# Kernel optimization log

Measured on AMD Instinct MI355X. Metric: run time of the kernel, lower is better.

Reference implementation:

```python
import jax, jax.numpy as jnp
import numpy as np

B, C, F, NH, DK, DV = 16, 256, 32, 8, 32, 64
S = F * F
EPS = 1e-5
SCALE = DK ** -0.5


def _bn(t, g, b, m, v):
    # t: [B, Ch, H, W]; eval-mode batchnorm with running stats
    inv = g / jnp.sqrt(v + EPS)
    return t * inv[None, :, None, None] + (b - m * inv)[None, :, None, None]


def setup_inputs() -> dict:
    key = jax.random.key(0)
    ks = jax.random.split(key, 24)
    n = lambda i, shape, s=0.05: jax.random.normal(ks[i], shape, jnp.float32) * s
    u = lambda i, shape: jax.random.uniform(ks[i], shape, jnp.float32, 0.5, 1.5)
    # relative-position index table (buffer)
    r = np.arange(F)
    pos = np.stack(np.meshgrid(r, r, indexing='ij'), axis=-1).reshape(-1, 2)
    rel = np.abs(pos[:, None, :] - pos[None, :, :])
    pos_indices = jnp.asarray(rel[..., 0] * F + rel[..., 1], jnp.int32)  # [S, S]
    return {
        'x': jax.random.normal(ks[0], (B, C, F, F), jnp.float32),
        'Wq': n(1, (NH * DK, C)), 'q_g': u(2, (NH * DK,)), 'q_b': n(3, (NH * DK,)), 'q_m': n(4, (NH * DK,)), 'q_v': u(5, (NH * DK,)),
        'Wk': n(6, (NH * DK, C)), 'k_g': u(7, (NH * DK,)), 'k_b': n(8, (NH * DK,)), 'k_m': n(9, (NH * DK,)), 'k_v': u(10, (NH * DK,)),
        'Wv': n(11, (NH * DV, C)), 'v_g': u(12, (NH * DV,)), 'v_b': n(13, (NH * DV,)), 'v_m': n(14, (NH * DV,)), 'v_v': u(15, (NH * DV,)),
        'pos_emb': n(16, (F * F, NH)),
        'Wo': n(17, (C, NH * DV)), 'bo': n(18, (C,)),
        'o_g': u(19, (C,)), 'o_b': n(20, (C,)), 'o_m': n(21, (C,)), 'o_v': u(22, (C,)),
        'pos_indices': pos_indices,
    }


def reference(x, Wq, q_g, q_b, q_m, q_v, Wk, k_g, k_b, k_m, k_v, Wv, v_g, v_b, v_m, v_v,
              pos_emb, Wo, bo, o_g, o_b, o_m, o_v, pos_indices):
    # 1x1 conv == channel GEMM
    q = _bn(jnp.einsum('bchw,oc->bohw', x, Wq), q_g, q_b, q_m, q_v)
    k = _bn(jnp.einsum('bchw,oc->bohw', x, Wk), k_g, k_b, k_m, k_v)
    v = _bn(jnp.einsum('bchw,oc->bohw', x, Wv), v_g, v_b, v_m, v_v)
    # b (n d) h w -> b n s d
    qh = q.reshape(B, NH, DK, S).transpose(0, 1, 3, 2)
    kh = k.reshape(B, NH, DK, S).transpose(0, 1, 3, 2)
    vh = v.reshape(B, NH, DV, S).transpose(0, 1, 3, 2)
    attn = jnp.einsum('bnqd,bnkd->bnqk', qh, kh) * SCALE  # [B, NH, S, S]
    bias = pos_emb[pos_indices]                            # [S, S, NH] gather
    attn = attn + jnp.transpose(bias, (2, 0, 1))[None] / SCALE
    attn = jax.nn.softmax(attn, axis=-1)
    o = jnp.einsum('bnqk,bnkd->bnqd', attn, vh)            # [B, NH, S, DV]
    o = o.transpose(0, 1, 3, 2).reshape(B, NH * DV, F, F)  # b (n d) h w
    o = jax.nn.gelu(o, approximate=False)                  # torch default GELU (erf)
    o = jnp.einsum('bchw,oc->bohw', o, Wo) + bo[None, :, None, None]
    return _bn(o, o_g, o_b, o_m, o_v)
```

## Files before the change

kernel.cpp:

```cpp
#include <hip/hip_runtime.h>

#define B_ 16
#define C_ 256
#define NH_ 8
#define DK_ 32
#define DV_ 64
#define S_ 1024
#define CV_ 512

typedef __bf16 bf16;
typedef bf16 bf16x4 __attribute__((ext_vector_type(4)));
typedef bf16 bf16x8 __attribute__((ext_vector_type(8)));
typedef float f32x4 __attribute__((ext_vector_type(4)));

constexpr float EPSV = 1e-5f;
constexpr float SCALE_ = 0.17677669529663687f;
constexpr float LOG2E_ = 1.4426950408889634f;
constexpr float QSCALE_ = SCALE_ * LOG2E_;
constexpr float BSCALE_ = (1.0f / SCALE_) * LOG2E_;

__global__ void prep_kernel(const float* __restrict__ Wq, const float* __restrict__ qg, const float* __restrict__ qb, const float* __restrict__ qm, const float* __restrict__ qv,
                            const float* __restrict__ Wk, const float* __restrict__ kg, const float* __restrict__ kb, const float* __restrict__ km, const float* __restrict__ kv,
                            const float* __restrict__ Wv, const float* __restrict__ vg, const float* __restrict__ vb, const float* __restrict__ vm, const float* __restrict__ vv,
                            const float* __restrict__ Wo, const float* __restrict__ bo, const float* __restrict__ og_, const float* __restrict__ ob_, const float* __restrict__ om_, const float* __restrict__ ov_,
                            bf16* __restrict__ wqkv, float* __restrict__ bqkv, bf16* __restrict__ wo2, float* __restrict__ bo2) {
  int idx = blockIdx.x * 256 + threadIdx.x;
  if (idx < 1024 * 256) {
    int o = idx >> 8, c = idx & 255;
    float w, g, v;
    if (o < 256)      { w = Wq[o * 256 + c];        g = qg[o];       v = qv[o]; }
    else if (o < 512) { w = Wk[(o - 256) * 256 + c]; g = kg[o - 256]; v = kv[o - 256]; }
    else              { w = Wv[(o - 512) * 256 + c]; g = vg[o - 512]; v = vv[o - 512]; }
    float inv = g * rsqrtf(v + EPSV);
    wqkv[idx] = (bf16)(w * inv);
    if (c == 0) {
      float bb, m;
      if (o < 256)      { bb = qb[o];       m = qm[o]; }
      else if (o < 512) { bb = kb[o - 256]; m = km[o - 256]; }
      else              { bb = vb[o - 512]; m = vm[o - 512]; }
      bqkv[o] = bb - m * inv;
    }
  } else {
    int j = idx - 1024 * 256;
    if (j < 256 * 512) {
      int co = j >> 9, cv = j & 511;
      float inv = og_[co] * rsqrtf(ov_[co] + EPSV);
      wo2[j] = (bf16)(Wo[j] * inv);
      if (cv == 0) bo2[co] = bo[co] * inv + ob_[co] - om_[co] * inv;
    }
  }
}

__global__ __launch_bounds__(256) void xpose_kernel(const float* __restrict__ x, bf16* __restrict__ xT) {
  __shared__ bf16 t[64][66];
  int b = blockIdx.z, c0 = blockIdx.y * 64, s0 = blockIdx.x * 64;
  const float* xp = x + ((size_t)b * C_ + c0) * S_ + s0;
#pragma unroll
  for (int p = 0; p < 4; ++p) {
    int q = p * 256 + threadIdx.x;
    int ci = q >> 4, si4 = (q & 15) * 4;
    float4 v = *(const float4*)(xp + (size_t)ci * S_ + si4);
    t[si4 + 0][ci] = (bf16)v.x;
    t[si4 + 1][ci] = (bf16)v.y;
    t[si4 + 2][ci] = (bf16)v.z;
    t[si4 + 3][ci] = (bf16)v.w;
  }
  __syncthreads();
  bf16* op = xT + ((size_t)b * S_ + s0) * C_ + c0;
#pragma unroll
  for (int p = 0; p < 4; ++p) {
    int q = p * 256 + threadIdx.x;
    int si = q >> 4, ci4 = (q & 15) * 4;
    bf16x4 pk;
#pragma unroll
    for (int e = 0; e < 4; ++e) pk[e] = t[si][ci4 + e];
    *(bf16x4*)(op + (size_t)si * C_ + ci4) = pk;
  }
}

__device__ __forceinline__ void gload16(const void* g, void* l) {
  __builtin_amdgcn_global_load_lds((const __attribute__((address_space(1))) void*)g,
                                   (__attribute__((address_space(3))) void*)l, 16, 0, 0);
}

__global__ __launch_bounds__(256) void qkv_gemm_kernel(const bf16* __restrict__ wqkv, const float* __restrict__ bqkv,
                                                       const bf16* __restrict__ xT, bf16* __restrict__ qh,
                                                       bf16* __restrict__ kh, bf16* __restrict__ vT) {
  __shared__ bf16 alds[2][128 * 32];
  __shared__ bf16 blds[2][128 * 32];
  const int b = blockIdx.z;
  const int ob = blockIdx.y * 128, sb = blockIdx.x * 128;
  const int w = threadIdx.x >> 6, lane = threadIdx.x & 63;
  const int g = lane >> 4, lo = lane & 15;
  const int ow = (w >> 1) * 64, sw = (w & 1) * 64;

  const int r0 = threadIdx.x >> 2, c4 = threadIdx.x & 3;
  const int swz = (c4 ^ ((r0 >> 1) & 3)) * 8;
  const bf16* aS = wqkv + (size_t)(ob + r0) * C_ + swz;
  const bf16* bS = xT + ((size_t)b * S_ + sb + r0) * C_ + swz;
  const int ldst = threadIdx.x * 8;
  auto stage = [&](int buf, int kc) {
    gload16(aS + kc, &alds[buf][ldst]);
    gload16(aS + (size_t)64 * C_ + kc, &alds[buf][ldst + 2048]);
    gload16(bS + kc, &blds[buf][ldst]);
    gload16(bS + (size_t)64 * C_ + kc, &blds[buf][ldst + 2048]);
  };

  f32x4 acc[4][4] = {};

  stage(0, 0);
  __syncthreads();

  for (int step = 0; step < 8; ++step) {
    const int cur = step & 1;
    if (step < 7) stage(cur ^ 1, (step + 1) * 32);
    bf16x8 af[4], bfr[4];
#pragma unroll
    for (int i = 0; i < 4; ++i) {
      const int row = ow + i * 16 + lo;
      const int ch = (g ^ ((lo >> 1) & 3)) * 8;
      af[i] = *(const bf16x8*)(&alds[cur][row * 32 + ch]);
    }
#pragma unroll
    for (int j = 0; j < 4; ++j) {
      const int row = sw + j * 16 + lo;
      const int ch = (g ^ ((lo >> 1) & 3)) * 8;
      bfr[j] = *(const bf16x8*)(&blds[cur][row * 32 + ch]);
    }
#pragma unroll
    for (int i = 0; i < 4; ++i)
#pragma unroll
      for (int j = 0; j < 4; ++j)
        acc[i][j] = __builtin_amdgcn_mfma_f32_16x16x32_bf16(af[i], bfr[j], acc[i][j], 0, 0, 0);
    __syncthreads();
  }

#pragma unroll
  for (int i = 0; i < 4; ++i) {
    const int o0 = ob + ow + i * 16 + 4 * g;
    const bool isv = o0 >= 512;
    const bool isq = o0 < 256;
    float bias4[4];
#pragma unroll
    for (int r = 0; r < 4; ++r) bias4[r] = bqkv[o0 + r];
#pragma unroll
    for (int j = 0; j < 4; ++j) {
      const int s = sb + sw + j * 16 + lo;
      if (!isv) {
        const int n = (o0 >> 5) & 7;
        const int d0 = o0 & 31;
        bf16x4 pk;
#pragma unroll
        for (int r = 0; r < 4; ++r) {
          float v = acc[i][j][r] + bias4[r];
          pk[r] = (bf16)(isq ? v * QSCALE_ : v);
        }
        bf16* dst = (isq ? qh : kh) + (((size_t)b * NH_ + n) * S_ + s) * DK_ + d0;
        *(bf16x4*)dst = pk;
      } else {
        const int o2 = o0 - 512;
        const int n = o2 >> 6, dv0 = o2 & 63;
#pragma unroll
        for (int r = 0; r < 4; ++r)
          vT[(((size_t)b * NH_ + n) * DV_ + dv0 + r) * S_ + s] = (bf16)(acc[i][j][r] + bias4[r]);
      }
    }
  }
}

__global__ __launch_bounds__(512, 4) void attn_kernel(const bf16* __restrict__ qh, const bf16* __restrict__ kh,
                                                      const bf16* __restrict__ vT, const float* __restrict__ pos_emb,
                                                      bf16* __restrict__ og) {
  __shared__ f32x4 E4[32][64];
  __shared__ bf16 klds[2][64 * 32];
  __shared__ bf16 vlds[2][64 * 64];
  const int n = blockIdx.x, qt = blockIdx.y, b = blockIdx.z;
  const int w = threadIdx.x >> 6, lane = threadIdx.x & 63;
  const int g = lane >> 4, lo = lane & 15;
  const size_t bn = (size_t)b * NH_ + n;
  const bf16* __restrict__ kbase = kh + bn * (size_t)S_ * DK_;
  const bf16* __restrict__ vbase = vT + bn * (size_t)DV_ * S_;

  const int krow = (w & 3) * 16 + (lane >> 2), kslot = lane & 3;
  const int vrow = w * 8 + (lane >> 3), vslot = lane & 7;
  const bf16* ksrc0 = kbase + (size_t)krow * DK_ + ((kslot ^ ((krow >> 2) & 3)) * 8);
  const bf16* vsrc0 = vbase + (size_t)vrow * S_ + ((vslot ^ (vrow & 7)) * 8);
  auto stage = [&](int buf, int kt) {
    if (w < 4) gload16(ksrc0 + (size_t)kt * DK_, &klds[buf][(w & 3) * 512]);
    gload16(vsrc0 + kt, &vlds[buf][w * 512]);
  };

  stage(0, 0);

  for (int i = threadIdx.x; i < 32 * 64; i += 512) {
    const int dr = i >> 6, d = i & 63;
    f32x4 v;
#pragma unroll
    for (int j = 0; j < 4; ++j) {
      int dc = d - 28 - j;
      dc = dc < 0 ? -dc : dc;
      dc = dc > 31 ? 31 : dc;
      v[j] = pos_emb[(dr * 32 + dc) * NH_ + n] * BSCALE_;
    }
    E4[dr][d] = v;
  }

  const int qbase = qt * 256 + w * 32;
  const int q0 = qbase + lo, q1 = qbase + 16 + lo;
  const bf16x8 qf0 = *(const bf16x8*)(qh + (bn * S_ + q0) * DK_ + 8 * g);
  const bf16x8 qf1 = *(const bf16x8*)(qh + (bn * S_ + q1) * DK_ + 8 * g);
  const int qr = qbase >> 5;
  const int i00m = 12 + lo - 4 * g;

  f32x4 acc[4][2] = {};
  f32x4 lac[2] = {};
  bf16x8 ones;
#pragma unroll
  for (int j = 0; j < 8; ++j) ones[j] = (bf16)1.0f;

  asm volatile("s_waitcnt vmcnt(0)" ::: "memory");
  __syncthreads();

  const f32x4* __restrict__ E4f = &E4[0][0];

  for (int it = 0; it < 16; ++it) {
    const int kt = it * 64;
    const int cur = it & 1;
    if (it < 15) stage(cur ^ 1, kt + 64);
    const bf16* kbuf = &klds[cur][0];
    const bf16* vbuf = &vlds[cur][0];

    int dq = qr - 2 * it;
    int dra = dq < 0 ? -dq : dq;
    int dqb = dq - 1;
    int drb = dqb < 0 ? -dqb : dqb;
    const f32x4* pa = E4f + dra * 64 + i00m;
    const f32x4* pbq = E4f + drb * 64 + i00m;
    const f32x4 W0a = pa[16], W0b = pbq[16];

    bf16x8 pb[2][2];
#pragma unroll
    for (int u = 0; u < 4; ++u) {
      const int row = u * 16 + lo;
      bf16x8 ka = *(const bf16x8*)(kbuf + row * 32 + ((8 * g) ^ (((row >> 2) & 3) << 3)));
      f32x4 c0, c1;
      if (u == 0)      { c0 = W0a;    c1 = pa[32]; }
      else if (u == 1) { c0 = pa[0];  c1 = W0a; }
      else if (u == 2) { c0 = W0b;    c1 = pbq[32]; }
      else             { c0 = pbq[0]; c1 = W0b; }
      f32x4 s0 = __builtin_amdgcn_mfma_f32_16x16x32_bf16(ka, qf0, c0, 0, 0, 0);
      f32x4 s1 = __builtin_amdgcn_mfma_f32_16x16x32_bf16(ka, qf1, c1, 0, 0, 0);
      const int cb = (u & 1) * 4;
      const int up = u >> 1;
#pragma unroll
      for (int r = 0; r < 4; ++r) {
        pb[0][up][cb + r] = (bf16)__builtin_amdgcn_exp2f(s0[r]);
        pb[1][up][cb + r] = (bf16)__builtin_amdgcn_exp2f(s1[r]);
      }
    }

    __builtin_amdgcn_s_setprio(1);
    lac[0] = __builtin_amdgcn_mfma_f32_16x16x32_bf16(ones, pb[0][0], lac[0], 0, 0, 0);
    lac[0] = __builtin_amdgcn_mfma_f32_16x16x32_bf16(ones, pb[0][1], lac[0], 0, 0, 0);
    lac[1] = __builtin_amdgcn_mfma_f32_16x16x32_bf16(ones, pb[1][0], lac[1], 0, 0, 0);
    lac[1] = __builtin_amdgcn_mfma_f32_16x16x32_bf16(ones, pb[1][1], lac[1], 0, 0, 0);

#pragma unroll
    for (int t = 0; t < 4; ++t) {
      const int row = t * 16 + lo;
      const int rsw = row & 7;
      const bf16* vrow_p = vbuf + row * 64 + 4 * (g & 1);
      const int ghalf = g >> 1;
#pragma unroll
      for (int up = 0; up < 2; ++up) {
        bf16x4 a0 = *(const bf16x4*)(vrow_p + ((((4 * up + 0) + ghalf) ^ rsw) << 3));
        bf16x4 a1 = *(const bf16x4*)(vrow_p + ((((4 * up + 2) + ghalf) ^ rsw) << 3));
        bf16x8 va = __builtin_shufflevector(a0, a1, 0, 1, 2, 3, 4, 5, 6, 7);
        acc[t][0] = __builtin_amdgcn_mfma_f32_16x16x32_bf16(va, pb[0][up], acc[t][0], 0, 0, 0);
        acc[t][1] = __builtin_amdgcn_mfma_f32_16x16x32_bf16(va, pb[1][up], acc[t][1], 0, 0, 0);
      }
    }
    __builtin_amdgcn_s_setprio(0);

    asm volatile("s_waitcnt vmcnt(0)" ::: "memory");
    __syncthreads();
  }

#pragma unroll
  for (int h = 0; h < 2; ++h) {
    const float rinv = __builtin_amdgcn_rcpf(lac[h][0]);
    const int qx = qbase + 16 * h + lo;
    bf16* op = og + ((size_t)b * S_ + qx) * CV_ + n * DV_;
#pragma unroll
    for (int t = 0; t < 4; ++t) {
      bf16x4 pk;
#pragma unroll
      for (int r = 0; r < 4; ++r) {
        float xo = acc[t][h][r] * rinv;
        pk[r] = (bf16)(0.5f * xo * (1.f + erff(xo * 0.70710678118654752f)));
      }
      *(bf16x4*)(op + t * 16 + 4 * g) = pk;
    }
  }
}

__global__ __launch_bounds__(512, 4) void out_gemm_kernel(const bf16* __restrict__ wo2, const float* __restrict__ bo2,
                                                          const bf16* __restrict__ og, float* __restrict__ out) {
  const int b = blockIdx.z;
  const int cb = blockIdx.y * 64, sb = blockIdx.x * 128;
  const int w = threadIdx.x >> 6, lane = threadIdx.x & 63;
  const int g = lane >> 4, lo = lane & 15;
  const int cw = cb + (w >> 2) * 32, sw = sb + (w & 3) * 32;
  f32x4 acc[2][2] = {};
  const bf16* aB = wo2 + (size_t)(cw + lo) * CV_ + 8 * g;
  const bf16* bB = og + ((size_t)b * S_ + sw + lo) * CV_ + 8 * g;
#pragma unroll 2
  for (int kc = 0; kc < CV_; kc += 32) {
    bf16x8 af[2], bfr[2];
#pragma unroll
    for (int i = 0; i < 2; ++i) af[i] = *(const bf16x8*)(aB + (size_t)i * 16 * CV_ + kc);
#pragma unroll
    for (int j = 0; j < 2; ++j) bfr[j] = *(const bf16x8*)(bB + (size_t)j * 16 * CV_ + kc);
#pragma unroll
    for (int i = 0; i < 2; ++i)
#pragma unroll
      for (int j = 0; j < 2; ++j)
        acc[i][j] = __builtin_amdgcn_mfma_f32_16x16x32_bf16(af[i], bfr[j], acc[i][j], 0, 0, 0);
  }
#pragma unroll
  for (int i = 0; i < 2; ++i) {
    const int c0 = cw + i * 16 + 4 * g;
    float bias4[4];
#pragma unroll
    for (int r = 0; r < 4; ++r) bias4[r] = bo2[c0 + r];
#pragma unroll
    for (int j = 0; j < 2; ++j) {
      const int s = sw + j * 16 + lo;
#pragma unroll
      for (int r = 0; r < 4; ++r)
        out[((size_t)b * C_ + c0 + r) * S_ + s] = acc[i][j][r] + bias4[r];
    }
  }
}

extern "C" void kernel_launch(void* const* d_in, const int* in_sizes, int n_in,
                              void* d_out, int out_size, void* d_ws, size_t ws_size,
                              hipStream_t stream) {
  (void)in_sizes; (void)n_in; (void)out_size; (void)ws_size;
  const float* x   = (const float*)d_in[0];
  const float* Wq  = (const float*)d_in[1];
  const float* qg  = (const float*)d_in[2];
  const float* qb  = (const float*)d_in[3];
  const float* qm  = (const float*)d_in[4];
  const float* qv  = (const float*)d_in[5];
  const float* Wk  = (const float*)d_in[6];
  const float* kg  = (const float*)d_in[7];
  const float* kb  = (const float*)d_in[8];
  const float* km  = (const float*)d_in[9];
  const float* kv  = (const float*)d_in[10];
  const float* Wv  = (const float*)d_in[11];
  const float* vg  = (const float*)d_in[12];
  const float* vb  = (const float*)d_in[13];
  const float* vm  = (const float*)d_in[14];
  const float* vv  = (const float*)d_in[15];
  const float* pos = (const float*)d_in[16];
  const float* Wo  = (const float*)d_in[17];
  const float* bo  = (const float*)d_in[18];
  const float* ogm = (const float*)d_in[19];
  const float* obt = (const float*)d_in[20];
  const float* omn = (const float*)d_in[21];
  const float* ovr = (const float*)d_in[22];
  float* out = (float*)d_out;

  char* ws = (char*)d_ws;
  size_t off = 0;
  auto take = [&](size_t bytes) { char* p = ws + off; off += (bytes + 255) & ~(size_t)255; return p; };
  bf16*  wqkv = (bf16*) take((size_t)1024 * 256 * 2);
  float* bqkv = (float*)take(1024 * 4);
  bf16*  wo2  = (bf16*) take((size_t)256 * 512 * 2);
  float* bo2  = (float*)take(256 * 4);
  bf16*  xT   = (bf16*) take((size_t)B_ * S_ * C_ * 2);
  bf16*  qhb  = (bf16*) take((size_t)B_ * NH_ * S_ * DK_ * 2);
  bf16*  khb  = (bf16*) take((size_t)B_ * NH_ * S_ * DK_ * 2);
  bf16*  vTb  = (bf16*) take((size_t)B_ * NH_ * DV_ * S_ * 2);
  bf16*  ogb  = (bf16*) take((size_t)B_ * S_ * CV_ * 2);

  prep_kernel<<<dim3(1536), dim3(256), 0, stream>>>(Wq, qg, qb, qm, qv, Wk, kg, kb, km, kv,
                                                    Wv, vg, vb, vm, vv, Wo, bo, ogm, obt, omn, ovr,
                                                    wqkv, bqkv, wo2, bo2);
  xpose_kernel<<<dim3(16, 4, 16), dim3(256), 0, stream>>>(x, xT);
  qkv_gemm_kernel<<<dim3(8, 8, 16), dim3(256), 0, stream>>>(wqkv, bqkv, xT, qhb, khb, vTb);
  attn_kernel<<<dim3(8, 4, 16), dim3(512), 0, stream>>>(qhb, khb, vTb, pos, ogb);
  out_gemm_kernel<<<dim3(8, 4, 16), dim3(512), 0, stream>>>(wo2, bo2, ogb, out);
}
```

Baseline: 108.0 us.

## Stage out-projection GEMM tiles through double-buffered swizzled LDS

The output projection GEMM drops its direct global-memory fragment loads in favour of the same double-buffered, XOR-swizzled LDS staging scheme the QKV GEMM uses. Blocks shrink from 512 to 256 threads, and each wave now computes a 32x64 tile instead of 32x32. Operands are shared across waves through LDS, cutting redundant global loads, at the cost of a barrier per K-step and more LDS use. A small cosmetic tidy of the QKV GEMM fragment loads is included.

```diff
diff --git a/kernel.cpp b/kernel.cpp
--- a/kernel.cpp
+++ b/kernel.cpp
@@ -115,18 +115,13 @@
     const int cur = step & 1;
     if (step < 7) stage(cur ^ 1, (step + 1) * 32);
     bf16x8 af[4], bfr[4];
-#pragma unroll
-    for (int i = 0; i < 4; ++i) {
-      const int row = ow + i * 16 + lo;
-      const int ch = (g ^ ((lo >> 1) & 3)) * 8;
-      af[i] = *(const bf16x8*)(&alds[cur][row * 32 + ch]);
-    }
-#pragma unroll
-    for (int j = 0; j < 4; ++j) {
-      const int row = sw + j * 16 + lo;
-      const int ch = (g ^ ((lo >> 1) & 3)) * 8;
-      bfr[j] = *(const bf16x8*)(&blds[cur][row * 32 + ch]);
-    }
+    const int ch = (g ^ ((lo >> 1) & 3)) * 8;
+#pragma unroll
+    for (int i = 0; i < 4; ++i)
+      af[i] = *(const bf16x8*)(&alds[cur][(ow + i * 16 + lo) * 32 + ch]);
+#pragma unroll
+    for (int j = 0; j < 4; ++j)
+      bfr[j] = *(const bf16x8*)(&blds[cur][(sw + j * 16 + lo) * 32 + ch]);
 #pragma unroll
     for (int i = 0; i < 4; ++i)
 #pragma unroll
@@ -304,38 +299,60 @@
   }
 }
 
-__global__ __launch_bounds__(512, 4) void out_gemm_kernel(const bf16* __restrict__ wo2, const float* __restrict__ bo2,
-                                                          const bf16* __restrict__ og, float* __restrict__ out) {
+__global__ __launch_bounds__(256) void out_gemm_kernel(const bf16* __restrict__ wo2, const float* __restrict__ bo2,
+                                                       const bf16* __restrict__ og, float* __restrict__ out) {
+  __shared__ bf16 alds[2][64 * 32];
+  __shared__ bf16 blds[2][128 * 32];
   const int b = blockIdx.z;
   const int cb = blockIdx.y * 64, sb = blockIdx.x * 128;
   const int w = threadIdx.x >> 6, lane = threadIdx.x & 63;
   const int g = lane >> 4, lo = lane & 15;
-  const int cw = cb + (w >> 2) * 32, sw = sb + (w & 3) * 32;
-  f32x4 acc[2][2] = {};
-  const bf16* aB = wo2 + (size_t)(cw + lo) * CV_ + 8 * g;
-  const bf16* bB = og + ((size_t)b * S_ + sw + lo) * CV_ + 8 * g;
-#pragma unroll 2
-  for (int kc = 0; kc < CV_; kc += 32) {
-    bf16x8 af[2], bfr[2];
-#pragma unroll
-    for (int i = 0; i < 2; ++i) af[i] = *(const bf16x8*)(aB + (size_t)i * 16 * CV_ + kc);
-#pragma unroll
-    for (int j = 0; j < 2; ++j) bfr[j] = *(const bf16x8*)(bB + (size_t)j * 16 * CV_ + kc);
+  const int cw = (w >> 1) * 32, sw = (w & 1) * 64;
+
+  const int r0 = threadIdx.x >> 2, c4 = threadIdx.x & 3;
+  const int swz = (c4 ^ ((r0 >> 1) & 3)) * 8;
+  const bf16* aS = wo2 + (size_t)(cb + r0) * CV_ + swz;
+  const bf16* bS = og + ((size_t)b * S_ + sb + r0) * CV_ + swz;
+  const int ldst = threadIdx.x * 8;
+  auto stage = [&](int buf, int kc) {
+    gload16(aS + kc, &alds[buf][ldst]);
+    gload16(bS + kc, &blds[buf][ldst]);
+    gload16(bS + (size_t)64 * CV_ + kc, &blds[buf][ldst + 2048]);
+  };
+
+  f32x4 acc[2][4] = {};
+
+  stage(0, 0);
+  __syncthreads();
+
+  for (int step = 0; step < 16; ++step) {
+    const int cur = step & 1;
+    if (step < 15) stage(cur ^ 1, (step + 1) * 32);
+    bf16x8 af[2], bfr[4];
+    const int ch = (g ^ ((lo >> 1) & 3)) * 8;
 #pragma unroll
     for (int i = 0; i < 2; ++i)
-#pragma unroll
-      for (int j = 0; j < 2; ++j)
+      af[i] = *(const bf16x8*)(&alds[cur][(cw + i * 16 + lo) * 32 + ch]);
+#pragma unroll
+    for (int j = 0; j < 4; ++j)
+      bfr[j] = *(const bf16x8*)(&blds[cur][(sw + j * 16 + lo) * 32 + ch]);
+#pragma unroll
+    for (int i = 0; i < 2; ++i)
+#pragma unroll
+      for (int j = 0; j < 4; ++j)
         acc[i][j] = __builtin_amdgcn_mfma_f32_16x16x32_bf16(af[i], bfr[j], acc[i][j], 0, 0, 0);
-  }
+    __syncthreads();
+  }
+
 #pragma unroll
   for (int i = 0; i < 2; ++i) {
-    const int c0 = cw + i * 16 + 4 * g;
+    const int c0 = cb + cw + i * 16 + 4 * g;
     float bias4[4];
 #pragma unroll
     for (int r = 0; r < 4; ++r) bias4[r] = bo2[c0 + r];
 #pragma unroll
-    for (int j = 0; j < 2; ++j) {
-      const int s = sw + j * 16 + lo;
+    for (int j = 0; j < 4; ++j) {
+      const int s = sb + sw + j * 16 + lo;
 #pragma unroll
       for (int r = 0; r < 4; ++r)
         out[((size_t)b * C_ + c0 + r) * S_ + s] = acc[i][j][r] + bias4[r];
@@ -391,5 +408,5 @@
   xpose_kernel<<<dim3(16, 4, 16), dim3(256), 0, stream>>>(x, xT);
   qkv_gemm_kernel<<<dim3(8, 8, 16), dim3(256), 0, stream>>>(wqkv, bqkv, xT, qhb, khb, vTb);
   attn_kernel<<<dim3(8, 4, 16), dim3(512), 0, stream>>>(qhb, khb, vTb, pos, ogb);
-  out_gemm_kernel<<<dim3(8, 4, 16), dim3(512), 0, stream>>>(wo2, bo2, ogb, out);
-}
+  out_gemm_kernel<<<dim3(8, 4, 16), dim3(256), 0, stream>>>(wo2, bo2, ogb, out);
+}
```

After: 90.38 us, median of 3. 16.3% less time.
